# Optimization experiments

Hardware: AMD Instinct MI355X
Metric: run time of the kernel (lower is better)

Reference implementation:

```python
import jax, jax.numpy as jnp
import numpy as np

INPUT_DIM, PROJ_DIM, HIDDEN = 1, 16, 32
B, T = 2048, 2048


def setup_inputs() -> dict:
    key = jax.random.key(0)
    ks = jax.random.split(key, 9)
    s_in = 1.0 / np.sqrt(INPUT_DIM)
    s_h = 1.0 / np.sqrt(HIDDEN)
    s_p = 1.0 / np.sqrt(PROJ_DIM)
    return {
        "x_seq": jax.random.normal(ks[0], (B, T, INPUT_DIM), dtype=jnp.float32),
        # input_linear: Linear(input_dim, proj_dim)
        "Wp": jax.random.uniform(ks[1], (PROJ_DIM, INPUT_DIM), minval=-s_in, maxval=s_in),
        "bp": jax.random.uniform(ks[2], (PROJ_DIM,), minval=-s_in, maxval=s_in),
        # LSTM weights (PyTorch gate order i,f,g,o)
        "W_ih": jax.random.uniform(ks[3], (4 * HIDDEN, PROJ_DIM), minval=-s_h, maxval=s_h),
        "W_hh": jax.random.uniform(ks[4], (4 * HIDDEN, HIDDEN), minval=-s_h, maxval=s_h),
        "b_ih": jax.random.uniform(ks[5], (4 * HIDDEN,), minval=-s_h, maxval=s_h),
        "b_hh": jax.random.uniform(ks[6], (4 * HIDDEN,), minval=-s_h, maxval=s_h),
        # output_linear: Linear(hidden, input_dim)
        "Wo": jax.random.uniform(ks[7], (INPUT_DIM, HIDDEN), minval=-s_h, maxval=s_h),
        "bo": jax.random.uniform(ks[8], (INPUT_DIM,), minval=-s_h, maxval=s_h),
    }


def reference(x_seq, Wp, bp, W_ih, W_hh, b_ih, b_hh, Wo, bo):
    H = W_hh.shape[1]
    b, t, _ = x_seq.shape
    # input projection for all timesteps at once (same math as per-step Linear)
    # then pre-apply W_ih: [B,T,4H]
    xp = jnp.einsum("bti,pi->btp", x_seq, Wp) + bp
    gates_x = jnp.einsum("btp,gp->btg", xp, W_ih) + b_ih + b_hh
    gates_x = jnp.transpose(gates_x, (1, 0, 2))  # [T,B,4H]

    def step(carry, gx):
        h, c = carry
        gates = gx + h @ W_hh.T  # [B,4H]
        i, f, g, o = jnp.split(gates, 4, axis=-1)
        i = jax.nn.sigmoid(i)
        f = jax.nn.sigmoid(f)
        g = jnp.tanh(g)
        o = jax.nn.sigmoid(o)
        c = f * c + i * g
        h = o * jnp.tanh(c)
        return (h, c), h

    h0 = jnp.zeros((b, H), dtype=x_seq.dtype)
    c0 = jnp.zeros((b, H), dtype=x_seq.dtype)
    (_, _), hs = jax.lax.scan(step, (h0, c0), gates_x)  # hs: [T,B,H]
    outputs = jnp.einsum("tbh,oh->bto", hs, Wo) + bo  # [B,T,input_dim]
    return outputs
```

## Files before the change

kernel.cpp:

```cpp
#include <hip/hip_runtime.h>


#define BB 2048
#define TT 2048
#define HH 32

typedef _Float16 h2 __attribute__((ext_vector_type(2)));
typedef unsigned int uint2v __attribute__((ext_vector_type(2)));

__device__ __forceinline__ float gate_eval(float x, float m, float a, float b) {
    float e = __builtin_amdgcn_exp2f(x * m);
    float r = __builtin_amdgcn_rcpf(1.0f + e);
    return fmaf(a, r, b);
}

template <int CTRL>
__device__ __forceinline__ float dpp_add(float v) {
    int s = __builtin_amdgcn_update_dpp(0, __float_as_int(v), CTRL, 0xf, 0xf, true);
    return v + __int_as_float(s);
}

struct HVec { h2 v[16]; };

__device__ __forceinline__ HVec gather_h(const _Float16* base) {
    const float4* p = (const float4*)base;
    float4 q0 = p[0], q1 = p[1], q2 = p[2], q3 = p[3];
    HVec r;
    r.v[0]  = __builtin_bit_cast(h2, q0.x); r.v[1]  = __builtin_bit_cast(h2, q0.y);
    r.v[2]  = __builtin_bit_cast(h2, q0.z); r.v[3]  = __builtin_bit_cast(h2, q0.w);
    r.v[4]  = __builtin_bit_cast(h2, q1.x); r.v[5]  = __builtin_bit_cast(h2, q1.y);
    r.v[6]  = __builtin_bit_cast(h2, q1.z); r.v[7]  = __builtin_bit_cast(h2, q1.w);
    r.v[8]  = __builtin_bit_cast(h2, q2.x); r.v[9]  = __builtin_bit_cast(h2, q2.y);
    r.v[10] = __builtin_bit_cast(h2, q2.z); r.v[11] = __builtin_bit_cast(h2, q2.w);
    r.v[12] = __builtin_bit_cast(h2, q3.x); r.v[13] = __builtin_bit_cast(h2, q3.y);
    r.v[14] = __builtin_bit_cast(h2, q3.z); r.v[15] = __builtin_bit_cast(h2, q3.w);
    return r;
}

__global__ __launch_bounds__(256) void lstm_fused_kernel(
    const float* __restrict__ x_seq,
    const float* __restrict__ Wp,
    const float* __restrict__ bp,
    const float* __restrict__ W_ih,
    const float* __restrict__ W_hh,
    const float* __restrict__ b_ih,
    const float* __restrict__ b_hh,
    const float* __restrict__ Wo,
    const float* __restrict__ bo,
    float* __restrict__ out)
{
    const int tid  = threadIdx.x;
    const int wave = tid >> 6;
    const int lane = tid & 63;
    const int half = lane >> 5;
    const int j    = lane & 31;
    const int b    = blockIdx.x * 4 + wave;

    const int rA = half * HH + j;
    const int rB = 2 * HH + half * HH + j;

    h2 wA[16], wB[16];
    {
        const float2* pA = (const float2*)(W_hh + rA * HH);
        const float2* pB = (const float2*)(W_hh + rB * HH);
#pragma unroll
        for (int k = 0; k < 16; ++k) {
            float2 a = pA[k], q = pB[k];
            wA[k].x = (_Float16)a.x; wA[k].y = (_Float16)a.y;
            wB[k].x = (_Float16)q.x; wB[k].y = (_Float16)q.y;
        }
    }

    float xA = 0.f, kA = 0.f, xB = 0.f, kB = 0.f;
#pragma unroll
    for (int p = 0; p < 16; ++p) {
        float wpv = Wp[p], bpv = bp[p];
        float wa = W_ih[rA * 16 + p], wb = W_ih[rB * 16 + p];
        xA = fmaf(wa, wpv, xA);  kA = fmaf(wa, bpv, kA);
        xB = fmaf(wb, wpv, xB);  kB = fmaf(wb, bpv, kB);
    }
    kA += b_ih[rA] + b_hh[rA];
    kB += b_ih[rB] + b_hh[rB];

    const float LOG2E = 1.44269504088896340736f;
    const float mB = half ? -LOG2E : -2.0f * LOG2E;
    const float aB = half ? 1.0f   : 2.0f;
    const float bB = half ? 0.0f   : -1.0f;

    const float woj = Wo[j];
    const float bo0 = bo[0];

    __shared__ __align__(16) _Float16 hsh[4][2][HH];
    _Float16* hbase = &hsh[wave][half][0];
    hbase[j] = (_Float16)0.0f;

    float c = 0.0f;
    const float* xp = x_seq + (size_t)b * TT;
    float* op = out + (size_t)b * TT;

    HVec hcur = gather_h(hbase);
    float4 x4 = *(const float4*)(xp);

    for (int t = 0; t < TT; t += 4) {
        const int tn = (t + 4 < TT) ? (t + 4) : t;
        float4 x4n = *(const float4*)(xp + tn);
        float outv[4];
#pragma unroll
        for (int u = 0; u < 4; ++u) {
            float xv = (u == 0) ? x4.x : (u == 1) ? x4.y : (u == 2) ? x4.z : x4.w;

            float sA0 = kA, sA1 = xv * xA;
            float sB0 = kB, sB1 = xv * xB;
#pragma unroll
            for (int k = 0; k < 16; k += 2) {
                h2 h0 = hcur.v[k], h1 = hcur.v[k + 1];
                sA0 = __builtin_amdgcn_fdot2(wA[k],     h0, sA0, false);
                sB0 = __builtin_amdgcn_fdot2(wB[k],     h0, sB0, false);
                sA1 = __builtin_amdgcn_fdot2(wA[k + 1], h1, sA1, false);
                sB1 = __builtin_amdgcn_fdot2(wB[k + 1], h1, sB1, false);
            }

            float Aact = gate_eval(sA0 + sA1, -LOG2E, 1.0f, 0.0f);
            float Bact = gate_eval(sB0 + sB1, mB, aB, bB);

            uint2v eA = __builtin_amdgcn_permlane32_swap(
                __float_as_uint(Aact), __float_as_uint(Aact), false, false);
            uint2v eB = __builtin_amdgcn_permlane32_swap(
                __float_as_uint(Bact), __float_as_uint(Bact), false, false);
            float iv = __uint_as_float(eA[0]);
            float fv = __uint_as_float(eA[1]);
            float gv = __uint_as_float(eB[0]);
            float ov = __uint_as_float(eB[1]);

            c = fmaf(fv, c, iv * gv);
            float th = gate_eval(c, -2.0f * LOG2E, 2.0f, -1.0f);
            float h = ov * th;

            hbase[j] = (_Float16)h;
            hcur = gather_h(hbase);

            float po = woj * h;
            po = dpp_add<0x111>(po);
            po = dpp_add<0x112>(po);
            po = dpp_add<0x114>(po);
            po = dpp_add<0x118>(po);
            po = dpp_add<0x142>(po);
            outv[u] = po + bo0;
        }
        if (lane == 31) {
            *(float4*)(op + t) = make_float4(outv[0], outv[1], outv[2], outv[3]);
        }
        x4 = x4n;
    }
}

extern "C" void kernel_launch(void* const* d_in, const int* in_sizes, int n_in,
                              void* d_out, int out_size, void* d_ws, size_t ws_size,
                              hipStream_t stream) {
    const float* x_seq = (const float*)d_in[0];
    const float* Wp    = (const float*)d_in[1];
    const float* bp    = (const float*)d_in[2];
    const float* W_ih  = (const float*)d_in[3];
    const float* W_hh  = (const float*)d_in[4];
    const float* b_ih  = (const float*)d_in[5];
    const float* b_hh  = (const float*)d_in[6];
    const float* Wo    = (const float*)d_in[7];
    const float* bo    = (const float*)d_in[8];
    float* out = (float*)d_out;

    dim3 grid(BB / 4);
    dim3 block(256);
    lstm_fused_kernel<<<grid, block, 0, stream>>>(
        x_seq, Wp, bp, W_ih, W_hh, b_ih, b_hh, Wo, bo, out);
}
```

Measured before the change: 783.2 us.

## Interleave two independent batch sequences per wave to hide recurrence latency

Each wave now advances two batch rows through the LSTM recurrence, interleaving their dot products, activations, lane swaps and LDS round-trips. The goal is to fill the latency of the serial per-timestep dependency chain with independent work and to reuse the register-resident W_hh weights across two sequences. The grid is halved to 256 blocks, which is about one block per CU on a 256-CU part and reduces the number of waves available to hide latency. Register pressure also rises.

```diff
diff --git a/kernel.cpp b/kernel.cpp
--- a/kernel.cpp
+++ b/kernel.cpp
@@ -54,7 +54,7 @@
     const int lane = tid & 63;
     const int half = lane >> 5;
     const int j    = lane & 31;
-    const int b    = blockIdx.x * 4 + wave;
+    const int b0   = blockIdx.x * 8 + wave * 2;
 
     const int rA = half * HH + j;
     const int rB = 2 * HH + half * HH + j;
@@ -71,16 +71,16 @@
         }
     }
 
-    float xA = 0.f, kA = 0.f, xB = 0.f, kB = 0.f;
+    float xA_ = 0.f, kA_ = 0.f, xB_ = 0.f, kB_ = 0.f;
 #pragma unroll
     for (int p = 0; p < 16; ++p) {
         float wpv = Wp[p], bpv = bp[p];
         float wa = W_ih[rA * 16 + p], wb = W_ih[rB * 16 + p];
-        xA = fmaf(wa, wpv, xA);  kA = fmaf(wa, bpv, kA);
-        xB = fmaf(wb, wpv, xB);  kB = fmaf(wb, bpv, kB);
+        xA_ = fmaf(wa, wpv, xA_);  kA_ = fmaf(wa, bpv, kA_);
+        xB_ = fmaf(wb, wpv, xB_);  kB_ = fmaf(wb, bpv, kB_);
     }
-    kA += b_ih[rA] + b_hh[rA];
-    kB += b_ih[rB] + b_hh[rB];
+    kA_ += b_ih[rA] + b_hh[rA];
+    kB_ += b_ih[rB] + b_hh[rB];
 
     const float LOG2E = 1.44269504088896340736f;
     const float mB = half ? -LOG2E : -2.0f * LOG2E;
@@ -90,67 +90,109 @@
     const float woj = Wo[j];
     const float bo0 = bo[0];
 
-    __shared__ __align__(16) _Float16 hsh[4][2][HH];
-    _Float16* hbase = &hsh[wave][half][0];
-    hbase[j] = (_Float16)0.0f;
-
-    float c = 0.0f;
-    const float* xp = x_seq + (size_t)b * TT;
-    float* op = out + (size_t)b * TT;
-
-    HVec hcur = gather_h(hbase);
-    float4 x4 = *(const float4*)(xp);
+    __shared__ __align__(16) _Float16 hsh[4][2][2][HH];
+    _Float16* baseA = &hsh[wave][0][half][0];
+    _Float16* baseB = &hsh[wave][1][half][0];
+    baseA[j] = (_Float16)0.0f;
+    baseB[j] = (_Float16)0.0f;
+
+    float cA = 0.0f, cB = 0.0f;
+    const float* xpA = x_seq + (size_t)b0 * TT;
+    const float* xpB = x_seq + (size_t)(b0 + 1) * TT;
+    float* opA = out + (size_t)b0 * TT;
+    float* opB = out + (size_t)(b0 + 1) * TT;
+
+    HVec vA = gather_h(baseA);
+    HVec vB = gather_h(baseB);
+    float4 x4A = *(const float4*)(xpA);
+    float4 x4B = *(const float4*)(xpB);
 
     for (int t = 0; t < TT; t += 4) {
         const int tn = (t + 4 < TT) ? (t + 4) : t;
-        float4 x4n = *(const float4*)(xp + tn);
-        float outv[4];
+        float4 x4An = *(const float4*)(xpA + tn);
+        float4 x4Bn = *(const float4*)(xpB + tn);
+        float outA[4], outB[4];
 #pragma unroll
         for (int u = 0; u < 4; ++u) {
-            float xv = (u == 0) ? x4.x : (u == 1) ? x4.y : (u == 2) ? x4.z : x4.w;
-
-            float sA0 = kA, sA1 = xv * xA;
-            float sB0 = kB, sB1 = xv * xB;
+            float xvA = (u == 0) ? x4A.x : (u == 1) ? x4A.y : (u == 2) ? x4A.z : x4A.w;
+            float xvB = (u == 0) ? x4B.x : (u == 1) ? x4B.y : (u == 2) ? x4B.z : x4B.w;
+
+            float sAa0 = kA_, sAa1 = xvA * xA_;
+            float sAb0 = kB_, sAb1 = xvA * xB_;
 #pragma unroll
             for (int k = 0; k < 16; k += 2) {
-                h2 h0 = hcur.v[k], h1 = hcur.v[k + 1];
-                sA0 = __builtin_amdgcn_fdot2(wA[k],     h0, sA0, false);
-                sB0 = __builtin_amdgcn_fdot2(wB[k],     h0, sB0, false);
-                sA1 = __builtin_amdgcn_fdot2(wA[k + 1], h1, sA1, false);
-                sB1 = __builtin_amdgcn_fdot2(wB[k + 1], h1, sB1, false);
+                h2 h0 = vA.v[k], h1 = vA.v[k + 1];
+                sAa0 = __builtin_amdgcn_fdot2(wA[k],     h0, sAa0, false);
+                sAb0 = __builtin_amdgcn_fdot2(wB[k],     h0, sAb0, false);
+                sAa1 = __builtin_amdgcn_fdot2(wA[k + 1], h1, sAa1, false);
+                sAb1 = __builtin_amdgcn_fdot2(wB[k + 1], h1, sAb1, false);
             }
-
-            float Aact = gate_eval(sA0 + sA1, -LOG2E, 1.0f, 0.0f);
-            float Bact = gate_eval(sB0 + sB1, mB, aB, bB);
-
-            uint2v eA = __builtin_amdgcn_permlane32_swap(
-                __float_as_uint(Aact), __float_as_uint(Aact), false, false);
-            uint2v eB = __builtin_amdgcn_permlane32_swap(
-                __float_as_uint(Bact), __float_as_uint(Bact), false, false);
-            float iv = __uint_as_float(eA[0]);
-            float fv = __uint_as_float(eA[1]);
-            float gv = __uint_as_float(eB[0]);
-            float ov = __uint_as_float(eB[1]);
-
-            c = fmaf(fv, c, iv * gv);
-            float th = gate_eval(c, -2.0f * LOG2E, 2.0f, -1.0f);
-            float h = ov * th;
-
-            hbase[j] = (_Float16)h;
-            hcur = gather_h(hbase);
-
-            float po = woj * h;
-            po = dpp_add<0x111>(po);
-            po = dpp_add<0x112>(po);
-            po = dpp_add<0x114>(po);
-            po = dpp_add<0x118>(po);
-            po = dpp_add<0x142>(po);
-            outv[u] = po + bo0;
+            float AactA = gate_eval(sAa0 + sAa1, -LOG2E, 1.0f, 0.0f);
+            float BactA = gate_eval(sAb0 + sAb1, mB, aB, bB);
+
+            float sBa0 = kA_, sBa1 = xvB * xA_;
+            float sBb0 = kB_, sBb1 = xvB * xB_;
+#pragma unroll
+            for (int k = 0; k < 16; k += 2) {
+                h2 h0 = vB.v[k], h1 = vB.v[k + 1];
+                sBa0 = __builtin_amdgcn_fdot2(wA[k],     h0, sBa0, false);
+                sBb0 = __builtin_amdgcn_fdot2(wB[k],     h0, sBb0, false);
+                sBa1 = __builtin_amdgcn_fdot2(wA[k + 1], h1, sBa1, false);
+                sBb1 = __builtin_amdgcn_fdot2(wB[k + 1], h1, sBb1, false);
+            }
+
+            uint2v eAA = __builtin_amdgcn_permlane32_swap(
+                __float_as_uint(AactA), __float_as_uint(AactA), false, false);
+            uint2v eBA = __builtin_amdgcn_permlane32_swap(
+                __float_as_uint(BactA), __float_as_uint(BactA), false, false);
+            float ivA = __uint_as_float(eAA[0]);
+            float fvA = __uint_as_float(eAA[1]);
+            float gvA = __uint_as_float(eBA[0]);
+            float ovA = __uint_as_float(eBA[1]);
+            cA = fmaf(fvA, cA, ivA * gvA);
+            float thA = gate_eval(cA, -2.0f * LOG2E, 2.0f, -1.0f);
+            float hAs = ovA * thA;
+            baseA[j] = (_Float16)hAs;
+            vA = gather_h(baseA);
+
+            float AactB = gate_eval(sBa0 + sBa1, -LOG2E, 1.0f, 0.0f);
+            float BactB = gate_eval(sBb0 + sBb1, mB, aB, bB);
+            uint2v eAB = __builtin_amdgcn_permlane32_swap(
+                __float_as_uint(AactB), __float_as_uint(AactB), false, false);
+            uint2v eBB = __builtin_amdgcn_permlane32_swap(
+                __float_as_uint(BactB), __float_as_uint(BactB), false, false);
+            float ivB = __uint_as_float(eAB[0]);
+            float fvB = __uint_as_float(eAB[1]);
+            float gvB = __uint_as_float(eBB[0]);
+            float ovB = __uint_as_float(eBB[1]);
+            cB = fmaf(fvB, cB, ivB * gvB);
+            float thB = gate_eval(cB, -2.0f * LOG2E, 2.0f, -1.0f);
+            float hBs = ovB * thB;
+            baseB[j] = (_Float16)hBs;
+            vB = gather_h(baseB);
+
+            float poA = woj * hAs;
+            poA = dpp_add<0x111>(poA);
+            poA = dpp_add<0x112>(poA);
+            poA = dpp_add<0x114>(poA);
+            poA = dpp_add<0x118>(poA);
+            poA = dpp_add<0x142>(poA);
+            outA[u] = poA + bo0;
+
+            float poB = woj * hBs;
+            poB = dpp_add<0x111>(poB);
+            poB = dpp_add<0x112>(poB);
+            poB = dpp_add<0x114>(poB);
+            poB = dpp_add<0x118>(poB);
+            poB = dpp_add<0x142>(poB);
+            outB[u] = poB + bo0;
         }
         if (lane == 31) {
-            *(float4*)(op + t) = make_float4(outv[0], outv[1], outv[2], outv[3]);
+            *(float4*)(opA + t) = make_float4(outA[0], outA[1], outA[2], outA[3]);
+            *(float4*)(opB + t) = make_float4(outB[0], outB[1], outB[2], outB[3]);
         }
-        x4 = x4n;
+        x4A = x4An;
+        x4B = x4Bn;
     }
 }
 
@@ -168,7 +210,7 @@
     const float* bo    = (const float*)d_in[8];
     float* out = (float*)d_out;
 
-    dim3 grid(BB / 4);
+    dim3 grid(BB / 8);
     dim3 block(256);
     lstm_fused_kernel<<<grid, block, 0, stream>>>(
         x_seq, Wp, bp, W_ih, W_hh, b_ih, b_hh, Wo, bo, out);
```

Measured after the change: 865.9 us. 10.6% more time.
